# Performance work log

Hardware: AMD Instinct MI355X
Metric: run time of the kernel (lower is better)

Reference implementation:

```python
import jax, jax.numpy as jnp
import numpy as np

N_NODES = 100000
N_EDGES = 1600000
INPUT_DIM, HIDDEN_DIM, OUTPUT_DIM = 128, 256, 2
BN_EPS = 1e-5


def setup_inputs() -> dict:
    key = jax.random.key(0)
    ks = jax.random.split(key, 8)
    x = jax.random.normal(ks[0], (N_NODES, INPUT_DIM), jnp.float32)
    edge_index = jax.random.randint(ks[1], (2, N_EDGES), 0, N_NODES, dtype=jnp.int32).astype(jnp.int64)
    # Glorot-ish init for GCNConv weights; PyG GCNConv has bias by default.
    def glorot(k, fan_in, fan_out):
        s = jnp.sqrt(6.0 / (fan_in + fan_out))
        return jax.random.uniform(k, (fan_in, fan_out), jnp.float32, -s, s)
    return {
        "x": x,
        "edge_index": edge_index,
        "W0": glorot(ks[2], INPUT_DIM, HIDDEN_DIM),
        "b0": jnp.zeros((HIDDEN_DIM,), jnp.float32),
        "W1": glorot(ks[3], HIDDEN_DIM, HIDDEN_DIM),
        "b1": jnp.zeros((HIDDEN_DIM,), jnp.float32),
        "W2": glorot(ks[4], HIDDEN_DIM, OUTPUT_DIM),
        "b2": jnp.zeros((OUTPUT_DIM,), jnp.float32),
        "gamma0": jnp.ones((HIDDEN_DIM,), jnp.float32),
        "beta0": jnp.zeros((HIDDEN_DIM,), jnp.float32),
        "gamma1": jnp.ones((HIDDEN_DIM,), jnp.float32),
        "beta1": jnp.zeros((HIDDEN_DIM,), jnp.float32),
    }


def _gcn_norm(edge_index, num_nodes):
    # PyG gcn_norm: add self-loops, deg over destination, D^-1/2 A_hat D^-1/2
    loop = jnp.arange(num_nodes, dtype=edge_index.dtype)
    src = jnp.concatenate([edge_index[0], loop])
    dst = jnp.concatenate([edge_index[1], loop])
    deg = jax.ops.segment_sum(jnp.ones_like(dst, jnp.float32), dst, num_segments=num_nodes)
    dinv = jax.lax.rsqrt(jnp.maximum(deg, 1.0))  # deg >= 1 due to self-loops
    norm = dinv[src] * dinv[dst]  # [E + N]
    return src, dst, norm


def _gcn_conv(x, W, b, src, dst, norm, num_nodes):
    h = x @ W                          # [N, out] dense GEMM first (PyG order)
    msg = h[src] * norm[:, None]       # gather + edge scale
    out = jax.ops.segment_sum(msg, dst, num_segments=num_nodes)  # scatter-add
    return out + b


def _batchnorm(x, gamma, beta):
    # training-mode BatchNorm1d over nodes (biased variance, as torch uses for normalization)
    mean = jnp.mean(x, axis=0)
    var = jnp.mean(jnp.square(x - mean), axis=0)
    return (x - mean) * jax.lax.rsqrt(var + BN_EPS) * gamma + beta


def reference(x, edge_index, W0, b0, W1, b1, W2, b2, gamma0, beta0, gamma1, beta1):
    n = x.shape[0]
    src, dst, norm = _gcn_norm(edge_index, n)
    h = _gcn_conv(x, W0, b0, src, dst, norm, n)
    h = jax.nn.relu(_batchnorm(h, gamma0, beta0))  # dropout is identity (eval / deterministic)
    h = _gcn_conv(h, W1, b1, src, dst, norm, n)
    h = jax.nn.relu(_batchnorm(h, gamma1, beta1))
    out = _gcn_conv(h, W2, b2, src, dst, norm, n)
    return out
```

## Files before the change

### kernel.cpp

```cpp
#include <hip/hip_runtime.h>
#include <hip/hip_fp16.h>
#include <type_traits>


#define BN_EPS 1e-5f

union HF4 { float4 f; __half2 h[4]; };
union HF2 { float2 f; __half2 h[2]; };

typedef __attribute__((ext_vector_type(8))) _Float16 f16x8;
typedef __attribute__((ext_vector_type(4))) float f32x4;

__global__ void detect_i64(const unsigned int* __restrict__ w, int* flag) {
  __shared__ unsigned int red[256];
  unsigned int v = 0;
  int t = threadIdx.x;
  for (int i = t; i < 1024; i += 256) v |= w[2 * i + 1];
  red[t] = v;
  __syncthreads();
  for (int s = 128; s > 0; s >>= 1) {
    if (t < s) red[t] |= red[t + s];
    __syncthreads();
  }
  if (t == 0) *flag = (red[0] == 0u) ? 1 : 0;
}

__global__ void deg_count(const unsigned int* __restrict__ w, const int* __restrict__ flag,
                          int* __restrict__ deg, int E) {
  int i = blockIdx.x * blockDim.x + threadIdx.x;
  if (i >= E) return;
  int f = *flag;
  int d = (int)(f ? w[2 * ((size_t)E + i)] : w[(size_t)E + i]);
  atomicAdd(&deg[d], 1);
}

__global__ void make_dinv(const int* __restrict__ deg, float* __restrict__ dinv,
                          float* __restrict__ stats, int N) {
  int i = blockIdx.x * blockDim.x + threadIdx.x;
  if (i < 512) stats[i] = 0.f;
  if (i < N) dinv[i] = rsqrtf((float)deg[i] + 1.0f);
}

__global__ void scan_partial(const int* __restrict__ deg, int* __restrict__ blksum, int N) {
  __shared__ int s[256];
  int b = blockIdx.x, t = threadIdx.x;
  int base = b * 1024 + t * 4;
  int v = 0;
#pragma unroll
  for (int k = 0; k < 4; ++k) {
    int i = base + k;
    if (i < N) v += deg[i];
  }
  s[t] = v;
  __syncthreads();
  for (int st = 128; st > 0; st >>= 1) {
    if (t < st) s[t] += s[t + st];
    __syncthreads();
  }
  if (t == 0) blksum[b] = s[0];
}

__global__ void scan_blk(int* __restrict__ blksum, int B) {
  __shared__ int s[256];
  int t = threadIdx.x;
  int v = (t < B) ? blksum[t] : 0;
  s[t] = v;
  __syncthreads();
  for (int off = 1; off < 256; off <<= 1) {
    int u = (t >= off) ? s[t - off] : 0;
    __syncthreads();
    s[t] += u;
    __syncthreads();
  }
  if (t < B) blksum[t] = s[t] - v;
}

__global__ void scan_final(const int* __restrict__ deg, const int* __restrict__ blkoff,
                           int* __restrict__ rowptr, int* __restrict__ fill, int N, int E) {
  __shared__ int s[256];
  int b = blockIdx.x, t = threadIdx.x;
  int base = b * 1024 + t * 4;
  int v[4];
  int sum = 0;
#pragma unroll
  for (int k = 0; k < 4; ++k) {
    int i = base + k;
    v[k] = (i < N) ? deg[i] : 0;
    sum += v[k];
  }
  s[t] = sum;
  __syncthreads();
  for (int off = 1; off < 256; off <<= 1) {
    int u = (t >= off) ? s[t - off] : 0;
    __syncthreads();
    s[t] += u;
    __syncthreads();
  }
  int ex = s[t] - sum + blkoff[b];
#pragma unroll
  for (int k = 0; k < 4; ++k) {
    int i = base + k;
    if (i < N) {
      rowptr[i] = ex;
      fill[i] = ex;
      ex += v[k];
    }
  }
  if (b == 0 && t == 0) rowptr[N] = E;
}

__global__ void csr_scatter(const unsigned int* __restrict__ w, const int* __restrict__ flag,
                            const float* __restrict__ dinv, int* __restrict__ fill,
                            int* __restrict__ col, float* __restrict__ wgt, int E) {
  int e = blockIdx.x * blockDim.x + threadIdx.x;
  if (e >= E) return;
  int f = *flag;
  int s = (int)(f ? w[2 * (size_t)e] : w[e]);
  int d = (int)(f ? w[2 * ((size_t)E + e)] : w[(size_t)E + e]);
  int slot = atomicAdd(&fill[d], 1);
  col[slot] = s;
  wgt[slot] = dinv[s] * dinv[d];
}

__global__ void f32_to_f16(const float4* __restrict__ in, float4* __restrict__ outh, long n8) {
  long t = (long)blockIdx.x * blockDim.x + threadIdx.x;
  if (t >= n8) return;
  float4 a = in[2 * t], b = in[2 * t + 1];
  HF4 o;
  o.h[0] = __floats2half2_rn(a.x, a.y);
  o.h[1] = __floats2half2_rn(a.z, a.w);
  o.h[2] = __floats2half2_rn(b.x, b.y);
  o.h[3] = __floats2half2_rn(b.z, b.w);
  outh[t] = o.f;
}

__global__ void pack_w2(const float* __restrict__ W0, const float* __restrict__ W1,
                        _Float16* __restrict__ W0p, _Float16* __restrict__ W1p) {
  int idx = blockIdx.x * blockDim.x + threadIdx.x;
  const float* W = (idx < 128 * 256) ? W0 : W1;
  _Float16* Wp = (idx < 128 * 256) ? W0p : W1p;
  int li = (idx < 128 * 256) ? idx : idx - 128 * 256;
  int k = li >> 8, n = li & 255;
  int kb = k >> 5, kk = k & 31, seg = kk >> 3, j = kk & 7;
  Wp[(((kb * 4 + seg) * 256) + n) * 8 + j] = (_Float16)W[li];
}

template <int LPN, bool BN>
__global__ void agg_gather_h(const float4* __restrict__ inh, float4* __restrict__ outh,
                             const int* __restrict__ rowptr, const int* __restrict__ col,
                             const float* __restrict__ wgt, const float* __restrict__ dinv,
                             const float* __restrict__ scale, const float* __restrict__ shift,
                             int N) {
  long g = (long)blockIdx.x * blockDim.x + threadIdx.x;
  int n = (int)(g / LPN);
  int lane = (int)(g & (LPN - 1));
  if (n >= N) return;
  float sc[8], sh[8];
  if (BN) {
    int c0 = lane * 8;
#pragma unroll
    for (int i = 0; i < 8; ++i) {
      sc[i] = scale[c0 + i];
      sh[i] = shift[c0 + i];
    }
  }
  auto xf = [&](const HF4& u, float* o) {
#pragma unroll
    for (int i = 0; i < 4; ++i) {
      float2 f = __half22float2(u.h[i]);
      o[2 * i] = f.x;
      o[2 * i + 1] = f.y;
    }
    if (BN) {
#pragma unroll
      for (int i = 0; i < 8; ++i) o[i] = fmaxf(o[i] * sc[i] + sh[i], 0.f);
    }
  };
  float ws = dinv[n];
  ws *= ws;
  float acc[8], v[8];
  {
    HF4 u;
    u.f = inh[(long)n * LPN + lane];
    xf(u, v);
#pragma unroll
    for (int i = 0; i < 8; ++i) acc[i] = ws * v[i];
  }
  int beg = rowptr[n], end = rowptr[n + 1];
  int j = beg;
  for (; j + 3 < end; j += 4) {
    int s0 = col[j], s1 = col[j + 1], s2 = col[j + 2], s3 = col[j + 3];
    float w0 = wgt[j], w1 = wgt[j + 1], w2 = wgt[j + 2], w3 = wgt[j + 3];
    HF4 a, b, c, d;
    a.f = inh[(long)s0 * LPN + lane];
    b.f = inh[(long)s1 * LPN + lane];
    c.f = inh[(long)s2 * LPN + lane];
    d.f = inh[(long)s3 * LPN + lane];
    float va[8], vb[8], vc[8], vd[8];
    xf(a, va); xf(b, vb); xf(c, vc); xf(d, vd);
#pragma unroll
    for (int i = 0; i < 8; ++i)
      acc[i] += w0 * va[i] + w1 * vb[i] + w2 * vc[i] + w3 * vd[i];
  }
  for (; j < end; ++j) {
    int s0 = col[j];
    float w0 = wgt[j];
    HF4 a;
    a.f = inh[(long)s0 * LPN + lane];
    float va[8];
    xf(a, va);
#pragma unroll
    for (int i = 0; i < 8; ++i) acc[i] += w0 * va[i];
  }
  HF4 o;
  o.h[0] = __floats2half2_rn(acc[0], acc[1]);
  o.h[1] = __floats2half2_rn(acc[2], acc[3]);
  o.h[2] = __floats2half2_rn(acc[4], acc[5]);
  o.h[3] = __floats2half2_rn(acc[6], acc[7]);
  outh[(long)n * LPN + lane] = o.f;
}

template <int K, int NC>
__global__ __launch_bounds__(256) void gemm_mfma(const _Float16* __restrict__ A,
                                                 const float4* __restrict__ Wpack,
                                                 _Float16* __restrict__ H,
                                                 float* __restrict__ gsum,
                                                 float* __restrict__ gsq, int M) {
  __shared__ float red0[NC];
  __shared__ float red1[NC];
  int tid = threadIdx.x;
  if (tid < NC) {
    red0[tid] = 0.f;
    red1[tid] = 0.f;
  }
  __syncthreads();
  int wave = tid >> 6;
  int lane = tid & 63;
  int row0 = (blockIdx.x * 4 + wave) * 32;
  bool active = row0 + 31 < M;
  int arow0 = active ? row0 : 0;
  int r = lane & 15;
  int seg = lane >> 4;
  f32x4 acc0[NC / 16], acc1[NC / 16];
#pragma unroll
  for (int t = 0; t < NC / 16; ++t) {
    acc0[t] = (f32x4){0.f, 0.f, 0.f, 0.f};
    acc1[t] = (f32x4){0.f, 0.f, 0.f, 0.f};
  }
  const _Float16* arowA = A + (long)(arow0 + r) * K;
  const _Float16* arowB = A + (long)(arow0 + 16 + r) * K;
#pragma unroll
  for (int k0 = 0; k0 < K; k0 += 32) {
    f16x8 af0 = *(const f16x8*)(arowA + k0 + seg * 8);
    f16x8 af1 = *(const f16x8*)(arowB + k0 + seg * 8);
    const float4* wp = Wpack + ((k0 >> 5) * 4 + seg) * NC;
#pragma unroll
    for (int t = 0; t < NC / 16; ++t) {
      f16x8 bf = *(const f16x8*)(wp + t * 16 + r);
      acc0[t] = __builtin_amdgcn_mfma_f32_16x16x32_f16(af0, bf, acc0[t], 0, 0, 0);
      acc1[t] = __builtin_amdgcn_mfma_f32_16x16x32_f16(af1, bf, acc1[t], 0, 0, 0);
    }
  }
#pragma unroll
  for (int t = 0; t < NC / 16; ++t) {
    int c = t * 16 + r;
    float s = 0.f, q = 0.f;
#pragma unroll
    for (int qq = 0; qq < 4; ++qq) {
      float v0 = acc0[t][qq], v1 = acc1[t][qq];
      s += v0 + v1;
      q += v0 * v0 + v1 * v1;
    }
    s += __shfl_xor(s, 16, 64);
    s += __shfl_xor(s, 32, 64);
    q += __shfl_xor(q, 16, 64);
    q += __shfl_xor(q, 32, 64);
    if (active) {
      if (seg == 0) {
        atomicAdd(&red0[c], s);
        atomicAdd(&red1[c], q);
      }
#pragma unroll
      for (int qq = 0; qq < 4; ++qq) {
        H[(long)(row0 + seg * 4 + qq) * NC + c] = (_Float16)acc0[t][qq];
        H[(long)(row0 + 16 + seg * 4 + qq) * NC + c] = (_Float16)acc1[t][qq];
      }
    }
  }
  __syncthreads();
  if (tid < NC) {
    atomicAdd(&gsum[tid], red0[tid]);
    atomicAdd(&gsq[tid], red1[tid]);
  }
}

__global__ void bn_finalize(float* __restrict__ gsum, float* __restrict__ gsq,
                            const float* __restrict__ gamma, const float* __restrict__ beta,
                            float* __restrict__ scale, float* __restrict__ shift, float invN) {
  int c = threadIdx.x;
  float mean = gsum[c] * invN;
  float var = fmaxf(gsq[c] * invN - mean * mean, 0.f);
  float sc = rsqrtf(var + BN_EPS) * gamma[c];
  scale[c] = sc;
  shift[c] = beta[c] - mean * sc;
  gsum[c] = 0.f;
  gsq[c] = 0.f;
}

__global__ void bn_apply_proj(const float4* __restrict__ h_in, const float* __restrict__ scale,
                              const float* __restrict__ shift, const float* __restrict__ W2,
                              float* __restrict__ P, int N) {
  int tid = threadIdx.x;
  int row = blockIdx.x * 8 + (tid >> 5);
  int lr = tid & 31;
  if (row >= N) return;
  HF4 u;
  u.f = h_in[(long)row * 32 + lr];
  int c0 = lr * 8;
  float s0 = 0.f, s1 = 0.f;
#pragma unroll
  for (int i = 0; i < 4; ++i) {
    float2 f = __half22float2(u.h[i]);
    int ca = c0 + 2 * i, cb = c0 + 2 * i + 1;
    float va = fmaxf(f.x * scale[ca] + shift[ca], 0.f);
    float vb = fmaxf(f.y * scale[cb] + shift[cb], 0.f);
    s0 += va * W2[2 * ca] + vb * W2[2 * cb];
    s1 += va * W2[2 * ca + 1] + vb * W2[2 * cb + 1];
  }
#pragma unroll
  for (int off = 16; off > 0; off >>= 1) {
    s0 += __shfl_down(s0, off, 32);
    s1 += __shfl_down(s1, off, 32);
  }
  if (lr == 0) {
    P[2 * row] = s0;
    P[2 * row + 1] = s1;
  }
}

__global__ void final_gather(const float* __restrict__ P, float* __restrict__ out,
                             const int* __restrict__ rowptr, const int* __restrict__ col,
                             const float* __restrict__ wgt, const float* __restrict__ dinv,
                             const float* __restrict__ b2, int N) {
  int n = blockIdx.x * blockDim.x + threadIdx.x;
  if (n >= N) return;
  float w = dinv[n] * dinv[n];
  float a0 = w * P[2 * n + 0];
  float a1 = w * P[2 * n + 1];
  int end = rowptr[n + 1];
  for (int j = rowptr[n]; j < end; ++j) {
    int s = col[j];
    float ww = wgt[j];
    a0 += ww * P[2 * s + 0];
    a1 += ww * P[2 * s + 1];
  }
  out[2 * n + 0] = a0 + b2[0];
  out[2 * n + 1] = a1 + b2[1];
}

extern "C" void kernel_launch(void* const* d_in, const int* in_sizes, int n_in,
                              void* d_out, int out_size, void* d_ws, size_t ws_size,
                              hipStream_t stream) {
  const float* x = (const float*)d_in[0];
  const unsigned int* eidx = (const unsigned int*)d_in[1];
  const float* W0 = (const float*)d_in[2];
  const float* W1 = (const float*)d_in[4];
  const float* W2 = (const float*)d_in[6];
  const float* b2 = (const float*)d_in[7];
  const float* gamma0 = (const float*)d_in[8];
  const float* beta0 = (const float*)d_in[9];
  const float* gamma1 = (const float*)d_in[10];
  const float* beta1 = (const float*)d_in[11];

  const int N = in_sizes[0] / 128;
  const int E = in_sizes[1] / 2;
  float* out = (float*)d_out;

  char* base = (char*)d_ws;
  size_t off = 0;
  auto alloc = [&](size_t bytes) {
    size_t o = off;
    off = (off + bytes + 255) & ~(size_t)255;
    return o;
  };
  const size_t o_col = alloc((size_t)E * 4);
  const size_t o_wgt = alloc((size_t)E * 4);
  const size_t o_rowptr = alloc((size_t)(N + 1) * 4);
  const size_t o_deg = alloc((size_t)N * 4);
  const size_t o_fill = alloc((size_t)N * 4);
  const size_t o_dinv = alloc((size_t)N * 4);
  const size_t o_blk = alloc(1024 * 4);
  const size_t o_flag = alloc(256);
  const size_t o_stats = alloc(4096);
  const size_t o_P = alloc((size_t)N * 2 * 4);
  const size_t o_W0p = alloc(128 * 256 * 2);
  const size_t o_W1p = alloc(256 * 256 * 2);
  const size_t o_H1 = alloc((size_t)N * 256 * 2);
  const size_t o_H2 = alloc((size_t)N * 256 * 2);

  int* col = (int*)(base + o_col);
  float* wgt = (float*)(base + o_wgt);
  int* rowptr = (int*)(base + o_rowptr);
  int* deg = (int*)(base + o_deg);
  int* fill = (int*)(base + o_fill);
  float* dinv = (float*)(base + o_dinv);
  int* blk = (int*)(base + o_blk);
  int* flag = (int*)(base + o_flag);
  float* gsum = (float*)(base + o_stats);
  float* gsq = gsum + 256;
  float* scale = gsum + 512;
  float* shift = gsum + 768;
  float* P = (float*)(base + o_P);
  _Float16* W0p = (_Float16*)(base + o_W0p);
  _Float16* W1p = (_Float16*)(base + o_W1p);
  float4* H1 = (float4*)(base + o_H1);
  float4* H2 = (float4*)(base + o_H2);

  auto cdiv = [](long a, long b) { return (int)((a + b - 1) / b); };
  const float invN = 1.0f / (float)N;
  const int B1 = cdiv(N, 1024);

  hipLaunchKernelGGL(detect_i64, dim3(1), dim3(256), 0, stream, eidx, flag);
  hipMemsetAsync(deg, 0, (size_t)N * 4, stream);
  hipLaunchKernelGGL(deg_count, dim3(cdiv(E, 256)), dim3(256), 0, stream, eidx, flag, deg, E);

  hipLaunchKernelGGL(make_dinv, dim3(cdiv(N, 256)), dim3(256), 0, stream, deg, dinv, gsum, N);
  hipLaunchKernelGGL(scan_partial, dim3(B1), dim3(256), 0, stream, deg, blk, N);
  hipLaunchKernelGGL(scan_blk, dim3(1), dim3(256), 0, stream, blk, B1);
  hipLaunchKernelGGL(scan_final, dim3(B1), dim3(256), 0, stream, deg, blk, rowptr, fill, N, E);
  hipLaunchKernelGGL(csr_scatter, dim3(cdiv(E, 256)), dim3(256), 0, stream, eidx, flag, dinv,
                     fill, col, wgt, E);
  hipLaunchKernelGGL(pack_w2, dim3(cdiv(384 * 256, 256)), dim3(256), 0, stream, W0, W1, W0p, W1p);
  hipLaunchKernelGGL(f32_to_f16, dim3(cdiv((long)N * 16, 256)), dim3(256), 0, stream,
                     (const float4*)x, H1, (long)N * 16);

  hipLaunchKernelGGL((agg_gather_h<16, false>), dim3(cdiv((long)N * 16, 256)), dim3(256), 0,
                     stream, H1, H2, rowptr, col, wgt, dinv, nullptr, nullptr, N);
  hipLaunchKernelGGL((gemm_mfma<128, 256>), dim3(cdiv(N, 128)), dim3(256), 0, stream,
                     (const _Float16*)H2, (const float4*)W0p, (_Float16*)H1, gsum, gsq, N);

  hipLaunchKernelGGL(bn_finalize, dim3(1), dim3(256), 0, stream, gsum, gsq, gamma0, beta0, scale,
                     shift, invN);

  hipLaunchKernelGGL((agg_gather_h<32, true>), dim3(cdiv((long)N * 32, 256)), dim3(256), 0,
                     stream, H1, H2, rowptr, col, wgt, dinv, scale, shift, N);
  hipLaunchKernelGGL((gemm_mfma<256, 256>), dim3(cdiv(N, 128)), dim3(256), 0, stream,
                     (const _Float16*)H2, (const float4*)W1p, (_Float16*)H1, gsum, gsq, N);

  hipLaunchKernelGGL(bn_finalize, dim3(1), dim3(256), 0, stream, gsum, gsq, gamma1, beta1, scale,
                     shift, invN);
  hipLaunchKernelGGL(bn_apply_proj, dim3(cdiv(N, 8)), dim3(256), 0, stream, (const float4*)H1,
                     scale, shift, W2, P, N);

  hipLaunchKernelGGL(final_gather, dim3(cdiv(N, 256)), dim3(256), 0, stream, P, out, rowptr, col,
                     wgt, dinv, b2, N);
}
```

Before: 594.8 us.

## Interleave CSR column and weight into int2 and pre-convert edge indices

Stores each CSR edge as one int2 (source index, weight bits) instead of separate col and wgt arrays, so each gather loop issues one 8-byte load per edge instead of two 4-byte loads. The degree-count kernel now also writes compact 32-bit src/dst arrays into the not-yet-used H2 buffer, so the CSR scatter reads those instead of re-decoding the int64 edge_index. This adds 12.8 MB of extra writes in the preprocessing pass. It relies on H2 being large enough to hold 2E ints and not being needed before csr_scatter finishes.

Result: faster. 554.1 us (-6.8%).

```diff
diff --git a/kernel.cpp b/kernel.cpp
--- a/kernel.cpp
+++ b/kernel.cpp
@@ -1,12 +1,10 @@
 #include <hip/hip_runtime.h>
 #include <hip/hip_fp16.h>
-#include <type_traits>
 
 
 #define BN_EPS 1e-5f
 
 union HF4 { float4 f; __half2 h[4]; };
-union HF2 { float2 f; __half2 h[2]; };
 
 typedef __attribute__((ext_vector_type(8))) _Float16 f16x8;
 typedef __attribute__((ext_vector_type(4))) float f32x4;
@@ -25,12 +23,16 @@
   if (t == 0) *flag = (red[0] == 0u) ? 1 : 0;
 }
 
-__global__ void deg_count(const unsigned int* __restrict__ w, const int* __restrict__ flag,
-                          int* __restrict__ deg, int E) {
+__global__ void convert_deg(const unsigned int* __restrict__ w, const int* __restrict__ flag,
+                            int* __restrict__ srcI, int* __restrict__ dstI,
+                            int* __restrict__ deg, int E) {
   int i = blockIdx.x * blockDim.x + threadIdx.x;
   if (i >= E) return;
   int f = *flag;
+  int s = (int)(f ? w[2 * (size_t)i] : w[i]);
   int d = (int)(f ? w[2 * ((size_t)E + i)] : w[(size_t)E + i]);
+  srcI[i] = s;
+  dstI[i] = d;
   atomicAdd(&deg[d], 1);
 }
 
@@ -109,17 +111,14 @@
   if (b == 0 && t == 0) rowptr[N] = E;
 }
 
-__global__ void csr_scatter(const unsigned int* __restrict__ w, const int* __restrict__ flag,
+__global__ void csr_scatter(const int* __restrict__ src, const int* __restrict__ dst,
                             const float* __restrict__ dinv, int* __restrict__ fill,
-                            int* __restrict__ col, float* __restrict__ wgt, int E) {
+                            int2* __restrict__ edge, int E) {
   int e = blockIdx.x * blockDim.x + threadIdx.x;
   if (e >= E) return;
-  int f = *flag;
-  int s = (int)(f ? w[2 * (size_t)e] : w[e]);
-  int d = (int)(f ? w[2 * ((size_t)E + e)] : w[(size_t)E + e]);
+  int s = src[e], d = dst[e];
   int slot = atomicAdd(&fill[d], 1);
-  col[slot] = s;
-  wgt[slot] = dinv[s] * dinv[d];
+  edge[slot] = make_int2(s, __float_as_int(dinv[s] * dinv[d]));
 }
 
 __global__ void f32_to_f16(const float4* __restrict__ in, float4* __restrict__ outh, long n8) {
@@ -147,8 +146,8 @@
 
 template <int LPN, bool BN>
 __global__ void agg_gather_h(const float4* __restrict__ inh, float4* __restrict__ outh,
-                             const int* __restrict__ rowptr, const int* __restrict__ col,
-                             const float* __restrict__ wgt, const float* __restrict__ dinv,
+                             const int* __restrict__ rowptr, const int2* __restrict__ edge,
+                             const float* __restrict__ dinv,
                              const float* __restrict__ scale, const float* __restrict__ shift,
                              int N) {
   long g = (long)blockIdx.x * blockDim.x + threadIdx.x;
@@ -189,13 +188,14 @@
   int beg = rowptr[n], end = rowptr[n + 1];
   int j = beg;
   for (; j + 3 < end; j += 4) {
-    int s0 = col[j], s1 = col[j + 1], s2 = col[j + 2], s3 = col[j + 3];
-    float w0 = wgt[j], w1 = wgt[j + 1], w2 = wgt[j + 2], w3 = wgt[j + 3];
+    int2 e0 = edge[j], e1 = edge[j + 1], e2 = edge[j + 2], e3 = edge[j + 3];
+    float w0 = __int_as_float(e0.y), w1 = __int_as_float(e1.y);
+    float w2 = __int_as_float(e2.y), w3 = __int_as_float(e3.y);
     HF4 a, b, c, d;
-    a.f = inh[(long)s0 * LPN + lane];
-    b.f = inh[(long)s1 * LPN + lane];
-    c.f = inh[(long)s2 * LPN + lane];
-    d.f = inh[(long)s3 * LPN + lane];
+    a.f = inh[(long)e0.x * LPN + lane];
+    b.f = inh[(long)e1.x * LPN + lane];
+    c.f = inh[(long)e2.x * LPN + lane];
+    d.f = inh[(long)e3.x * LPN + lane];
     float va[8], vb[8], vc[8], vd[8];
     xf(a, va); xf(b, vb); xf(c, vc); xf(d, vd);
 #pragma unroll
@@ -203,10 +203,10 @@
       acc[i] += w0 * va[i] + w1 * vb[i] + w2 * vc[i] + w3 * vd[i];
   }
   for (; j < end; ++j) {
-    int s0 = col[j];
-    float w0 = wgt[j];
+    int2 e0 = edge[j];
+    float w0 = __int_as_float(e0.y);
     HF4 a;
-    a.f = inh[(long)s0 * LPN + lane];
+    a.f = inh[(long)e0.x * LPN + lane];
     float va[8];
     xf(a, va);
 #pragma unroll
@@ -339,9 +339,9 @@
 }
 
 __global__ void final_gather(const float* __restrict__ P, float* __restrict__ out,
-                             const int* __restrict__ rowptr, const int* __restrict__ col,
-                             const float* __restrict__ wgt, const float* __restrict__ dinv,
-                             const float* __restrict__ b2, int N) {
+                             const int* __restrict__ rowptr, const int2* __restrict__ edge,
+                             const float* __restrict__ dinv, const float* __restrict__ b2,
+                             int N) {
   int n = blockIdx.x * blockDim.x + threadIdx.x;
   if (n >= N) return;
   float w = dinv[n] * dinv[n];
@@ -349,10 +349,10 @@
   float a1 = w * P[2 * n + 1];
   int end = rowptr[n + 1];
   for (int j = rowptr[n]; j < end; ++j) {
-    int s = col[j];
-    float ww = wgt[j];
-    a0 += ww * P[2 * s + 0];
-    a1 += ww * P[2 * s + 1];
+    int2 e = edge[j];
+    float ww = __int_as_float(e.y);
+    a0 += ww * P[2 * e.x + 0];
+    a1 += ww * P[2 * e.x + 1];
   }
   out[2 * n + 0] = a0 + b2[0];
   out[2 * n + 1] = a1 + b2[1];
@@ -383,8 +383,7 @@
     off = (off + bytes + 255) & ~(size_t)255;
     return o;
   };
-  const size_t o_col = alloc((size_t)E * 4);
-  const size_t o_wgt = alloc((size_t)E * 4);
+  const size_t o_edge = alloc((size_t)E * 8);
   const size_t o_rowptr = alloc((size_t)(N + 1) * 4);
   const size_t o_deg = alloc((size_t)N * 4);
   const size_t o_fill = alloc((size_t)N * 4);
@@ -398,8 +397,7 @@
   const size_t o_H1 = alloc((size_t)N * 256 * 2);
   const size_t o_H2 = alloc((size_t)N * 256 * 2);
 
-  int* col = (int*)(base + o_col);
-  float* wgt = (float*)(base + o_wgt);
+  int2* edge = (int2*)(base + o_edge);
   int* rowptr = (int*)(base + o_rowptr);
   int* deg = (int*)(base + o_deg);
   int* fill = (int*)(base + o_fill);
@@ -415,6 +413,9 @@
   _Float16* W1p = (_Float16*)(base + o_W1p);
   float4* H1 = (float4*)(base + o_H1);
   float4* H2 = (float4*)(base + o_H2);
+  int* idx32 = (int*)(base + o_H2);
+  int* srcI = idx32;
+  int* dstI = idx32 + E;
 
   auto cdiv = [](long a, long b) { return (int)((a + b - 1) / b); };
   const float invN = 1.0f / (float)N;
@@ -422,20 +423,21 @@
 
   hipLaunchKernelGGL(detect_i64, dim3(1), dim3(256), 0, stream, eidx, flag);
   hipMemsetAsync(deg, 0, (size_t)N * 4, stream);
-  hipLaunchKernelGGL(deg_count, dim3(cdiv(E, 256)), dim3(256), 0, stream, eidx, flag, deg, E);
+  hipLaunchKernelGGL(convert_deg, dim3(cdiv(E, 256)), dim3(256), 0, stream, eidx, flag, srcI,
+                     dstI, deg, E);
 
   hipLaunchKernelGGL(make_dinv, dim3(cdiv(N, 256)), dim3(256), 0, stream, deg, dinv, gsum, N);
   hipLaunchKernelGGL(scan_partial, dim3(B1), dim3(256), 0, stream, deg, blk, N);
   hipLaunchKernelGGL(scan_blk, dim3(1), dim3(256), 0, stream, blk, B1);
   hipLaunchKernelGGL(scan_final, dim3(B1), dim3(256), 0, stream, deg, blk, rowptr, fill, N, E);
-  hipLaunchKernelGGL(csr_scatter, dim3(cdiv(E, 256)), dim3(256), 0, stream, eidx, flag, dinv,
-                     fill, col, wgt, E);
+  hipLaunchKernelGGL(csr_scatter, dim3(cdiv(E, 256)), dim3(256), 0, stream, srcI, dstI, dinv,
+                     fill, edge, E);
   hipLaunchKernelGGL(pack_w2, dim3(cdiv(384 * 256, 256)), dim3(256), 0, stream, W0, W1, W0p, W1p);
   hipLaunchKernelGGL(f32_to_f16, dim3(cdiv((long)N * 16, 256)), dim3(256), 0, stream,
                      (const float4*)x, H1, (long)N * 16);
 
   hipLaunchKernelGGL((agg_gather_h<16, false>), dim3(cdiv((long)N * 16, 256)), dim3(256), 0,
-                     stream, H1, H2, rowptr, col, wgt, dinv, nullptr, nullptr, N);
+                     stream, H1, H2, rowptr, edge, dinv, nullptr, nullptr, N);
   hipLaunchKernelGGL((gemm_mfma<128, 256>), dim3(cdiv(N, 128)), dim3(256), 0, stream,
                      (const _Float16*)H2, (const float4*)W0p, (_Float16*)H1, gsum, gsq, N);
 
@@ -443,7 +445,7 @@
                      shift, invN);
 
   hipLaunchKernelGGL((agg_gather_h<32, true>), dim3(cdiv((long)N * 32, 256)), dim3(256), 0,
-                     stream, H1, H2, rowptr, col, wgt, dinv, scale, shift, N);
+                     stream, H1, H2, rowptr, edge, dinv, scale, shift, N);
   hipLaunchKernelGGL((gemm_mfma<256, 256>), dim3(cdiv(N, 128)), dim3(256), 0, stream,
                      (const _Float16*)H2, (const float4*)W1p, (_Float16*)H1, gsum, gsq, N);
 
@@ -452,6 +454,6 @@
   hipLaunchKernelGGL(bn_apply_proj, dim3(cdiv(N, 8)), dim3(256), 0, stream, (const float4*)H1,
                      scale, shift, W2, P, N);
 
-  hipLaunchKernelGGL(final_gather, dim3(cdiv(N, 256)), dim3(256), 0, stream, P, out, rowptr, col,
-                     wgt, dinv, b2, N);
-}
+  hipLaunchKernelGGL(final_gather, dim3(cdiv(N, 256)), dim3(256), 0, stream, P, out, rowptr,
+                     edge, dinv, b2, N);
+}
```
